# Kernel optimization log

Measured on AMD Instinct MI355X. Metric: run time of the kernel, lower is better.

Reference implementation:

```python
import jax, jax.numpy as jnp
import numpy as np

jax.config.update("jax_enable_x64", True)

P = 2013265921          # NTT-friendly prime 15 * 2**27 + 1 (int64-safe proxy for BLS12-377 Fr)
GEN = 31                # generator of the multiplicative group of F_P
LOGN = 22
N = 1 << LOGN           # domain_size
C = 4                   # columns, as in the module docstring example


def _pow_table(base, n):
    """powers[k] = base**k mod P for k in [0, n), built by repeated doubling (vectorized)."""
    pw = np.ones(n, dtype=np.int64)
    cur = base % P
    step = 1
    while step < n:
        hi = min(2 * step, n)
        pw[step:hi] = (pw[:hi - step] * cur) % P
        cur = (cur * cur) % P
        step *= 2
    return pw


def setup_inputs() -> dict:
    key = jax.random.key(0)
    x = jax.random.randint(key, (N, C), 0, P, dtype=jnp.int64)
    omega = pow(GEN, (P - 1) // N, P)          # primitive N-th root of unity
    omega_inv = pow(omega, P - 2, P)           # its inverse (Fermat)
    twiddles = jnp.asarray(_pow_table(omega_inv, N // 2))  # omega_inv**k, k < N/2  (the 'Params' table)
    n_inv = jnp.asarray(pow(N, P - 2, P), dtype=jnp.int64)  # N^{-1} mod P
    return {"input": x, "twiddles": twiddles, "n_inv": n_inv}


def reference(input, twiddles, n_inv):
    """Inverse NTT over F_P, columns transformed independently. Output in natural order."""
    n, c = input.shape
    logn = n.bit_length() - 1
    # bit-reversal permutation indices (static; computed with numpy)
    idx = np.arange(n)
    rev = np.zeros(n, dtype=np.int64)
    for i in range(logn):
        rev = (rev << 1) | ((idx >> i) & 1)
    x = input[rev]
    # iterative Cooley-Tukey butterflies, logn stages
    for s in range(1, logn + 1):
        m = 1 << s
        half = m >> 1
        w = twiddles[:: n // m]                 # [half] = omega_inv**(j * n/m)
        xr = x.reshape(-1, m, c)                # [n/m, m, c]
        lo, hi = xr[:, :half], xr[:, half:]
        t = (w[None, :, None] * hi) % P         # modular twiddle multiply
        x = jnp.concatenate([(lo + t) % P, (lo - t) % P], axis=1).reshape(n, c)
    return (x * n_inv) % P                      # scale by N^{-1}
```

## Files before the change

### kernel.cpp

```cpp
#include <hip/hip_runtime.h>
#include <stdint.h>

static constexpr uint32_t P = 2013265921u;
static constexpr int      LOGM = 11;
static constexpr int      MSZ  = 1 << LOGM;
static constexpr uint32_t NHALF = 1u << 21;

__host__ __device__ constexpr uint32_t neg_pinv32() {
    uint32_t x = 1u;
    for (int i = 0; i < 5; ++i) x *= 2u - P * x;
    return 0u - x;
}
static constexpr uint32_t NEG_PINV = neg_pinv32();
static constexpr uint32_t R1 = (uint32_t)(((uint64_t)1 << 32) % P);
static constexpr uint32_t R2 = (uint32_t)(((uint64_t)R1 * R1) % P);

__device__ __forceinline__ uint32_t mont_mul(uint32_t a, uint32_t b) {
    uint64_t t = (uint64_t)a * (uint64_t)b;
    uint32_t m = (uint32_t)t * NEG_PINV;
    uint32_t r = (uint32_t)((t + (uint64_t)m * P) >> 32);
    return r >= P ? r - P : r;
}
__device__ __forceinline__ uint32_t to_mont(uint32_t a) { return mont_mul(a, R2); }
__device__ __forceinline__ uint32_t add_p(uint32_t a, uint32_t b) {
    uint32_t r = a + b; return r >= P ? r - P : r;
}
__device__ __forceinline__ uint32_t sub_p(uint32_t a, uint32_t b) {
    return a >= b ? a - b : a + P - b;
}

__global__ void build_rtab(const uint32_t* __restrict__ tw, uint32_t* __restrict__ rtab_g) {
    int e = threadIdx.x;
    if (e < MSZ / 2) rtab_g[e] = to_mont(tw[(uint32_t)e << LOGM]);
}

template <bool PASS2>
__global__ __launch_bounds__(256) void intt_pass(
        const uint4* src, uint4* dst,
        const uint32_t* __restrict__ tw,
        const uint32_t* __restrict__ rtab_g,
        const uint32_t* __restrict__ ninv_p)
{
    __shared__ uint4    buf[MSZ];
    __shared__ uint32_t rtab[MSZ / 2];

    const int      tid = threadIdx.x;
    const uint32_t bid = blockIdx.x;
    const uint32_t col = ((bid & 7u) << 8) | (bid >> 3);

    for (int e = tid; e < MSZ / 2; e += 256) rtab[e] = rtab_g[e];

#pragma unroll
    for (int r = 0; r < 8; ++r) {
        int p = tid + (r << 8);
        uint32_t rv = __brev((uint32_t)p) >> (32 - LOGM);
        buf[p] = src[rv * (uint32_t)MSZ + col];
    }
    __syncthreads();

    for (int s = 1; s <= LOGM; ++s) {
        const int half = 1 << (s - 1);
#pragma unroll
        for (int r = 0; r < 4; ++r) {
            int b  = tid + (r << 8);
            int j  = b & (half - 1);
            int lo = ((b >> (s - 1)) << s) | j;
            int hi = lo + half;
            uint32_t wm = rtab[j << (LOGM - s)];
            uint4 L = buf[lo];
            uint4 H = buf[hi];
            uint32_t tx = mont_mul(wm, H.x);
            uint32_t ty = mont_mul(wm, H.y);
            uint32_t tz = mont_mul(wm, H.z);
            uint32_t tww = mont_mul(wm, H.w);
            buf[lo] = make_uint4(add_p(L.x, tx), add_p(L.y, ty),
                                 add_p(L.z, tz), add_p(L.w, tww));
            buf[hi] = make_uint4(sub_p(L.x, tx), sub_p(L.y, ty),
                                 sub_p(L.z, tz), sub_p(L.w, tww));
        }
        __syncthreads();
    }

    if (!PASS2) {
        uint32_t tm   = to_mont(tw[col * (uint32_t)tid]);
        uint32_t step = to_mont(tw[col << 8]);
#pragma unroll
        for (int r = 0; r < 8; ++r) {
            int k2 = tid + (r << 8);
            uint4 v = buf[k2];
            dst[col * (uint32_t)MSZ + (uint32_t)k2] =
                make_uint4(mont_mul(tm, v.x), mont_mul(tm, v.y),
                           mont_mul(tm, v.z), mont_mul(tm, v.w));
            tm = mont_mul(tm, step);
        }
    } else {
        uint32_t nm = to_mont(*ninv_p);
#pragma unroll
        for (int r = 0; r < 8; ++r) {
            int k1 = tid + (r << 8);
            uint4 v = buf[k1];
            dst[(uint32_t)k1 * (uint32_t)MSZ + col] =
                make_uint4(mont_mul(nm, v.x), mont_mul(nm, v.y),
                           mont_mul(nm, v.z), mont_mul(nm, v.w));
        }
    }
}

extern "C" void kernel_launch(void* const* d_in, const int* in_sizes, int n_in,
                              void* d_out, int out_size, void* d_ws, size_t ws_size,
                              hipStream_t stream)
{
    const uint4*    x    = (const uint4*)d_in[0];
    const uint32_t* tw   = (const uint32_t*)d_in[1];
    const uint32_t* ninv = (const uint32_t*)d_in[2];
    uint4*          out  = (uint4*)d_out;
    uint32_t*       rtab_g = (uint32_t*)d_ws;

    build_rtab<<<dim3(1), dim3(1024), 0, stream>>>(tw, rtab_g);
    intt_pass<false><<<dim3(2048), dim3(256), 0, stream>>>(x, out, tw, rtab_g, ninv);
    intt_pass<true ><<<dim3(2048), dim3(256), 0, stream>>>(out, out, tw, rtab_g, ninv);
}
```

Baseline: 234.9 us.

## Restructure in-block NTT into register radix-8 stages with swizzled shared memory

Replaces the eleven shared-memory radix-2 stages per pass with three register-resident radix-8 stages and a final radix-4 stage fused into the twiddle/scale store. This cuts shared-memory round trips and barriers from eleven to four per pass. It adds an XOR swizzle on shared indices to avoid bank conflicts. Each block now builds its own twiddle table, removing the separate build_rtab launch, and the modular add, sub and reduce use branchless select forms. Register pressure rises, and the launch bound now asks for four blocks per SM.

```diff
diff --git a/kernel.cpp b/kernel.cpp
--- a/kernel.cpp
+++ b/kernel.cpp
@@ -4,7 +4,6 @@
 static constexpr uint32_t P = 2013265921u;
 static constexpr int      LOGM = 11;
 static constexpr int      MSZ  = 1 << LOGM;
-static constexpr uint32_t NHALF = 1u << 21;
 
 __host__ __device__ constexpr uint32_t neg_pinv32() {
     uint32_t x = 1u;
@@ -19,26 +18,47 @@
     uint64_t t = (uint64_t)a * (uint64_t)b;
     uint32_t m = (uint32_t)t * NEG_PINV;
     uint32_t r = (uint32_t)((t + (uint64_t)m * P) >> 32);
-    return r >= P ? r - P : r;
+    uint32_t s = r - P;
+    return s < r ? s : r;
 }
 __device__ __forceinline__ uint32_t to_mont(uint32_t a) { return mont_mul(a, R2); }
 __device__ __forceinline__ uint32_t add_p(uint32_t a, uint32_t b) {
-    uint32_t r = a + b; return r >= P ? r - P : r;
+    uint32_t r = a + b, s = r - P; return s < r ? s : r;
 }
 __device__ __forceinline__ uint32_t sub_p(uint32_t a, uint32_t b) {
-    return a >= b ? a - b : a + P - b;
+    uint32_t r = a - b, s = r + P; return s < r ? s : r;
 }
 
-__global__ void build_rtab(const uint32_t* __restrict__ tw, uint32_t* __restrict__ rtab_g) {
-    int e = threadIdx.x;
-    if (e < MSZ / 2) rtab_g[e] = to_mont(tw[(uint32_t)e << LOGM]);
+__device__ __forceinline__ uint4 mm4(uint32_t w, uint4 v) {
+    return make_uint4(mont_mul(w, v.x), mont_mul(w, v.y),
+                      mont_mul(w, v.z), mont_mul(w, v.w));
+}
+__device__ __forceinline__ void bf4(uint4& L, uint4& H, uint32_t w) {
+    uint4 t = mm4(w, H);
+    uint4 l = L;
+    L = make_uint4(add_p(l.x, t.x), add_p(l.y, t.y), add_p(l.z, t.z), add_p(l.w, t.w));
+    H = make_uint4(sub_p(l.x, t.x), sub_p(l.y, t.y), sub_p(l.z, t.z), sub_p(l.w, t.w));
+}
+
+__device__ __forceinline__ int fmap(int i) {
+    return i ^ (((i >> 3) ^ (i >> 6)) & 7);
+}
+
+__device__ __forceinline__ void radix8(uint4 x[8],
+        uint32_t ta, uint32_t tb0, uint32_t tb1,
+        uint32_t tc0, uint32_t tc1, uint32_t tc2, uint32_t tc3) {
+    bf4(x[0], x[1], ta);  bf4(x[2], x[3], ta);
+    bf4(x[4], x[5], ta);  bf4(x[6], x[7], ta);
+    bf4(x[0], x[2], tb0); bf4(x[1], x[3], tb1);
+    bf4(x[4], x[6], tb0); bf4(x[5], x[7], tb1);
+    bf4(x[0], x[4], tc0); bf4(x[1], x[5], tc1);
+    bf4(x[2], x[6], tc2); bf4(x[3], x[7], tc3);
 }
 
 template <bool PASS2>
-__global__ __launch_bounds__(256) void intt_pass(
-        const uint4* src, uint4* dst,
+__global__ __launch_bounds__(256, 4) void intt_pass(
+        const uint4* __restrict__ src, uint4* __restrict__ dst,
         const uint32_t* __restrict__ tw,
-        const uint32_t* __restrict__ rtab_g,
         const uint32_t* __restrict__ ninv_p)
 {
     __shared__ uint4    buf[MSZ];
@@ -48,60 +68,82 @@
     const uint32_t bid = blockIdx.x;
     const uint32_t col = ((bid & 7u) << 8) | (bid >> 3);
 
-    for (int e = tid; e < MSZ / 2; e += 256) rtab[e] = rtab_g[e];
+    uint32_t tv[4];
+#pragma unroll
+    for (int j = 0; j < 4; ++j)
+        tv[j] = tw[(uint32_t)(tid + 256 * j) << LOGM];
 
+    const uint32_t r8 = __brev((uint32_t)tid) >> 24;
+    uint4 x[8];
 #pragma unroll
-    for (int r = 0; r < 8; ++r) {
-        int p = tid + (r << 8);
-        uint32_t rv = __brev((uint32_t)p) >> (32 - LOGM);
-        buf[p] = src[rv * (uint32_t)MSZ + col];
+    for (int m = 0; m < 8; ++m) {
+        uint32_t r3 = __brev((uint32_t)m) >> 29;
+        x[m] = src[((r3 << 8) | r8) * (uint32_t)MSZ + col];
+    }
+#pragma unroll
+    for (int j = 0; j < 4; ++j)
+        rtab[tid + 256 * j] = to_mont(tv[j]);
+    __syncthreads();
+
+    radix8(x, rtab[0], rtab[0], rtab[512],
+              rtab[0], rtab[256], rtab[512], rtab[768]);
+#pragma unroll
+    for (int m = 0; m < 8; ++m) buf[fmap(8 * tid + m)] = x[m];
+    __syncthreads();
+
+    {
+        const int L = tid & 7, hi = tid >> 3;
+        const int base = (hi << 6) | L;
+#pragma unroll
+        for (int m = 0; m < 8; ++m) x[m] = buf[fmap(base | (m << 3))];
+        radix8(x, rtab[L << 7],
+                  rtab[L << 6], rtab[(L << 6) + 512],
+                  rtab[L << 5], rtab[(L << 5) + 256],
+                  rtab[(L << 5) + 512], rtab[(L << 5) + 768]);
+#pragma unroll
+        for (int m = 0; m < 8; ++m) buf[fmap(base | (m << 3))] = x[m];
     }
     __syncthreads();
 
-    for (int s = 1; s <= LOGM; ++s) {
-        const int half = 1 << (s - 1);
+    {
+        const int L = tid & 63, hi = tid >> 6;
+        const int base = (hi << 9) | L;
 #pragma unroll
-        for (int r = 0; r < 4; ++r) {
-            int b  = tid + (r << 8);
-            int j  = b & (half - 1);
-            int lo = ((b >> (s - 1)) << s) | j;
-            int hi = lo + half;
-            uint32_t wm = rtab[j << (LOGM - s)];
-            uint4 L = buf[lo];
-            uint4 H = buf[hi];
-            uint32_t tx = mont_mul(wm, H.x);
-            uint32_t ty = mont_mul(wm, H.y);
-            uint32_t tz = mont_mul(wm, H.z);
-            uint32_t tww = mont_mul(wm, H.w);
-            buf[lo] = make_uint4(add_p(L.x, tx), add_p(L.y, ty),
-                                 add_p(L.z, tz), add_p(L.w, tww));
-            buf[hi] = make_uint4(sub_p(L.x, tx), sub_p(L.y, ty),
-                                 sub_p(L.z, tz), sub_p(L.w, tww));
-        }
-        __syncthreads();
+        for (int m = 0; m < 8; ++m) x[m] = buf[fmap(base | (m << 6))];
+        radix8(x, rtab[L << 4],
+                  rtab[L << 3], rtab[(L << 3) + 512],
+                  rtab[L << 2], rtab[(L << 2) + 256],
+                  rtab[(L << 2) + 512], rtab[(L << 2) + 768]);
+#pragma unroll
+        for (int m = 0; m < 8; ++m) buf[fmap(base | (m << 6))] = x[m];
     }
+    __syncthreads();
 
-    if (!PASS2) {
-        uint32_t tm   = to_mont(tw[col * (uint32_t)tid]);
-        uint32_t step = to_mont(tw[col << 8]);
+    const uint32_t nm   = PASS2 ? to_mont(*ninv_p) : 0u;
+    const uint32_t step = PASS2 ? 0u : to_mont(tw[col << 9]);
 #pragma unroll
-        for (int r = 0; r < 8; ++r) {
-            int k2 = tid + (r << 8);
-            uint4 v = buf[k2];
-            dst[col * (uint32_t)MSZ + (uint32_t)k2] =
-                make_uint4(mont_mul(tm, v.x), mont_mul(tm, v.y),
-                           mont_mul(tm, v.z), mont_mul(tm, v.w));
-            tm = mont_mul(tm, step);
-        }
-    } else {
-        uint32_t nm = to_mont(*ninv_p);
+    for (int g = 0; g < 2; ++g) {
+        const int lo = tid + (g << 8);
+        uint4 y[4];
 #pragma unroll
-        for (int r = 0; r < 8; ++r) {
-            int k1 = tid + (r << 8);
-            uint4 v = buf[k1];
-            dst[(uint32_t)k1 * (uint32_t)MSZ + col] =
-                make_uint4(mont_mul(nm, v.x), mont_mul(nm, v.y),
-                           mont_mul(nm, v.z), mont_mul(nm, v.w));
+        for (int m = 0; m < 4; ++m) y[m] = buf[fmap(lo | (m << 9))];
+        const uint32_t t10  = rtab[lo << 1];
+        const uint32_t t110 = rtab[lo];
+        const uint32_t t111 = rtab[lo + 512];
+        bf4(y[0], y[1], t10);  bf4(y[2], y[3], t10);
+        bf4(y[0], y[2], t110); bf4(y[1], y[3], t111);
+
+        if (!PASS2) {
+            uint32_t tm = to_mont(tw[col * (uint32_t)lo]);
+#pragma unroll
+            for (int m = 0; m < 4; ++m) {
+                dst[col * (uint32_t)MSZ + (uint32_t)((m << 9) | lo)] = mm4(tm, y[m]);
+                tm = mont_mul(tm, step);
+            }
+        } else {
+#pragma unroll
+            for (int m = 0; m < 4; ++m)
+                dst[(uint32_t)((m << 9) | lo) * (uint32_t)MSZ + col] = mm4(nm, y[m]);
         }
     }
 }
@@ -114,9 +156,7 @@
     const uint32_t* tw   = (const uint32_t*)d_in[1];
     const uint32_t* ninv = (const uint32_t*)d_in[2];
     uint4*          out  = (uint4*)d_out;
-    uint32_t*       rtab_g = (uint32_t*)d_ws;
 
-    build_rtab<<<dim3(1), dim3(1024), 0, stream>>>(tw, rtab_g);
-    intt_pass<false><<<dim3(2048), dim3(256), 0, stream>>>(x, out, tw, rtab_g, ninv);
-    intt_pass<true ><<<dim3(2048), dim3(256), 0, stream>>>(out, out, tw, rtab_g, ninv);
+    intt_pass<false><<<dim3(2048), dim3(256), 0, stream>>>(x, out, tw, ninv);
+    intt_pass<true ><<<dim3(2048), dim3(256), 0, stream>>>(out, out, tw, ninv);
 }
```

After: 216.5 us. 1.08x faster.
